# Kernel tuning notes

Measured on AMD Instinct MI355X. Metric: run time of the kernel, lower is better.

Reference implementation:

```python
import jax, jax.numpy as jnp
import numpy as np

N_NODES = 100000
N_EDGES = 1600000
N_REL = 8
IN_CH = 128
HID = 64
OUT_CH = 128


def _rgcn_layer(x, src, dst, et, W_rel, W_root, b, num_rel):
    # x: [N, Fin]; W_rel: [R, Fin, Fout]; W_root: [Fin, Fout]; b: [Fout]
    N = x.shape[0]
    # Transform once per relation, then gather per edge (avoids per-edge matmul)
    xt = jnp.einsum('ni,rio->rno', x, W_rel)          # [R, N, Fout]
    msgs = xt[et, src]                                 # [E, Fout]
    # Per-(dst, relation) mean normalization (PyG RGCNConv aggr='mean' per relation)
    seg = dst * num_rel + et                           # combined segment id
    deg = jax.ops.segment_sum(jnp.ones_like(et, dtype=x.dtype), seg,
                              num_segments=N * num_rel)  # [N*R]
    norm = 1.0 / jnp.maximum(deg[seg], 1.0)            # [E]
    agg = jax.ops.segment_sum(msgs * norm[:, None], dst, num_segments=N)  # [N, Fout]
    return agg + x @ W_root + b


def setup_inputs() -> dict:
    key = jax.random.key(0)
    ks = jax.random.split(key, 9)
    x = jax.random.normal(ks[0], (N_NODES, IN_CH), dtype=jnp.float32)
    edge_index = jax.random.randint(ks[1], (2, N_EDGES), 0, N_NODES, dtype=jnp.int64)
    edge_type = jax.random.randint(ks[2], (N_EDGES,), 0, N_REL, dtype=jnp.int64)
    s1 = 1.0 / np.sqrt(IN_CH)
    s2 = 1.0 / np.sqrt(HID)
    W1 = jax.random.uniform(ks[3], (N_REL, IN_CH, HID), jnp.float32, -s1, s1)
    root1 = jax.random.uniform(ks[4], (IN_CH, HID), jnp.float32, -s1, s1)
    b1 = jnp.zeros((HID,), jnp.float32)
    W2 = jax.random.uniform(ks[5], (N_REL, HID, OUT_CH), jnp.float32, -s2, s2)
    root2 = jax.random.uniform(ks[6], (HID, OUT_CH), jnp.float32, -s2, s2)
    b2 = jnp.zeros((OUT_CH,), jnp.float32)
    return {"x": x, "edge_index": edge_index, "edge_type": edge_type,
            "W1": W1, "root1": root1, "b1": b1,
            "W2": W2, "root2": root2, "b2": b2}


def reference(x, edge_index, edge_type, W1, root1, b1, W2, root2, b2):
    src, dst = edge_index[0], edge_index[1]
    h = _rgcn_layer(x, src, dst, edge_type, W1, root1, b1, N_REL)
    h = jax.nn.relu(h)
    out = _rgcn_layer(h, src, dst, edge_type, W2, root2, b2, N_REL)
    return out
```

## Files before the change

### kernel.cpp

```cpp
#include <hip/hip_runtime.h>
#include <cstdint>
#include <cstddef>

#define NREL 8

typedef __attribute__((ext_vector_type(8))) short bfrag8;
typedef __attribute__((ext_vector_type(4))) float facc4;

__device__ __forceinline__ ushort f2bf(float f) {
  union { float f; uint u; } v; v.f = f;
  uint u = v.u + 0x7fffu + ((v.u >> 16) & 1u);
  return (ushort)(u >> 16);
}
__device__ __forceinline__ float bf2f(ushort u) {
  union { uint u; float f; } v; v.u = ((uint)u) << 16;
  return v.f;
}
__device__ __forceinline__ float readlane_f(float v, int l) {
  union { float f; int i; } u; u.f = v;
  u.i = __builtin_amdgcn_readlane(u.i, l);
  return u.f;
}

__global__ __launch_bounds__(256) void cvt_all_kernel(const float* __restrict__ W1,
                                                      const float* __restrict__ r1,
                                                      const float* __restrict__ W2,
                                                      const float* __restrict__ r2,
                                                      ushort* __restrict__ W1t,
                                                      ushort* __restrict__ r1t,
                                                      ushort* __restrict__ W2t,
                                                      ushort* __restrict__ r2t) {
  int idx = blockIdx.x * 256 + threadIdx.x;
  const float* in; ushort* out; int K, N, rel;
  if (idx < 65536)        { in = W1; out = W1t; K = 128; N = 64;  rel = idx >> 13; idx &= 8191; }
  else if (idx < 73728)   { idx -= 65536; in = r1; out = r1t; K = 128; N = 64; rel = 0; }
  else if (idx < 139264)  { idx -= 73728; in = W2; out = W2t; K = 64; N = 128; rel = idx >> 13; idx &= 8191; }
  else if (idx < 147456)  { idx -= 139264; in = r2; out = r2t; K = 64; N = 128; rel = 0; }
  else return;
  int n = idx / K, k = idx - n * K;
  out[(size_t)rel * K * N + (size_t)n * K + k] =
      f2bf(in[(size_t)rel * K * N + (size_t)k * N + n]);
}

__global__ __launch_bounds__(256) void fused1_kernel(const float* __restrict__ x,
                                                     const ushort* __restrict__ W1t,
                                                     ushort* __restrict__ xt,
                                                     const int* __restrict__ dst,
                                                     const int* __restrict__ et,
                                                     uint* __restrict__ hist,
                                                     uint* __restrict__ rank,
                                                     int M, int E, int HB) {
  __shared__ __align__(16) ushort Axs[64][136];
  __shared__ __align__(16) ushort Bws[64][136];
  const int bid = blockIdx.x;
  const int hq = bid / 3;
  if ((bid % 3) == 0 && hq < HB) {
    int base = (hq * 256 + threadIdx.x) * 8;
    if (base + 8 <= E) {
      int4 d0 = *(const int4*)&dst[base], d1 = *(const int4*)&dst[base + 4];
      int4 r0 = *(const int4*)&et[base],  r1 = *(const int4*)&et[base + 4];
      int dd[8] = {d0.x, d0.y, d0.z, d0.w, d1.x, d1.y, d1.z, d1.w};
      int rr[8] = {r0.x, r0.y, r0.z, r0.w, r1.x, r1.y, r1.z, r1.w};
      uint rk[8];
#pragma unroll
      for (int j = 0; j < 8; ++j)
        rk[j] = atomicAdd(&hist[(size_t)rr[j] * M + dd[j]], 1u);
      *(uint4*)&rank[base] = make_uint4(rk[0], rk[1], rk[2], rk[3]);
      *(uint4*)&rank[base + 4] = make_uint4(rk[4], rk[5], rk[6], rk[7]);
    } else {
      for (int j = 0; base + j < E; ++j)
        rank[base + j] = atomicAdd(&hist[(size_t)et[base + j] * M + dst[base + j]], 1u);
    }
    return;
  }
  const int gidx = (hq < HB) ? (bid - hq - 1) : (bid - HB);
  const int tid = threadIdx.x;
  const int w = tid >> 6, l = tid & 63;
  const int rows0 = gidx * 64;
#pragma unroll
  for (int i = 0; i < 8; ++i) {
    int g = tid + 256 * i;
    int row = g >> 5, c4 = (g & 31) * 4;
    int rr = rows0 + row; if (rr >= M) rr = M - 1;
    float4 v = *(const float4*)&x[(size_t)rr * 128 + c4];
    *(ushort4*)&Axs[row][c4] = make_ushort4(f2bf(v.x), f2bf(v.y), f2bf(v.z), f2bf(v.w));
  }
  __syncthreads();
  const int mrow = w * 16 + (l & 15);
  const int koff = (l >> 4) * 8;
  bfrag8 xf[4];
#pragma unroll
  for (int kc = 0; kc < 4; ++kc)
    xf[kc] = *(const bfrag8*)&Axs[mrow][kc * 32 + koff];
  const int m = rows0 + mrow;
  for (int r = 0; r < NREL; ++r) {
    __syncthreads();
#pragma unroll
    for (int i = 0; i < 8; ++i) {
      int g = tid + 256 * i;
      int row = g >> 5, c4 = (g & 31) * 4;
      *(ushort4*)&Bws[row][c4] = *(const ushort4*)&W1t[((size_t)r * 64 + row) * 128 + c4];
    }
    __syncthreads();
#pragma unroll
    for (int ct = 0; ct < 4; ++ct) {
      facc4 acc = {0.f, 0.f, 0.f, 0.f};
#pragma unroll
      for (int kc = 0; kc < 4; ++kc) {
        bfrag8 af = *(const bfrag8*)&Bws[ct * 16 + (l & 15)][kc * 32 + koff];
        acc = __builtin_amdgcn_mfma_f32_16x16x32_bf16(af, xf[kc], acc, 0, 0, 0);
      }
      if (m < M) {
        int n0 = ct * 16 + (l >> 4) * 4;
        *(ushort4*)&xt[(size_t)m * 512 + r * 64 + n0] =
            make_ushort4(f2bf(acc[0]), f2bf(acc[1]), f2bf(acc[2]), f2bf(acc[3]));
      }
    }
  }
}

__global__ __launch_bounds__(256) void scan1_kernel(const uint* __restrict__ hist,
                                                    uint* __restrict__ bsum, int M) {
  __shared__ uint r[256];
  int b = blockIdx.x, t = threadIdx.x;
  int d = b * 256 + t;
  uint s = 0;
  if (d < M) {
#pragma unroll
    for (int i = 0; i < 8; ++i) s += hist[(size_t)i * M + d];
  }
  r[t] = s; __syncthreads();
  for (int dd = 128; dd > 0; dd >>= 1) { if (t < dd) r[t] += r[t + dd]; __syncthreads(); }
  if (t == 0) bsum[b] = r[0];
}

__global__ __launch_bounds__(512) void scan2_kernel(uint* __restrict__ bsum, int nb) {
  __shared__ uint s[512];
  int t = threadIdx.x;
  uint v = (t < nb) ? bsum[t] : 0u;
  s[t] = v;
  __syncthreads();
  for (int d = 1; d < 512; d <<= 1) {
    uint add = (t >= d) ? s[t - d] : 0u;
    __syncthreads();
    s[t] += add;
    __syncthreads();
  }
  if (t < nb) bsum[t] = s[t] - v;
}

__global__ __launch_bounds__(256) void scan3_kernel(const uint* __restrict__ hist,
                                                    const uint* __restrict__ bsum,
                                                    uint* __restrict__ off,
                                                    float* __restrict__ idg,
                                                    int M, int E) {
  __shared__ uint ts[256];
  int b = blockIdx.x, t = threadIdx.x;
  int d = b * 256 + t;
  uint h[8]; uint sum = 0;
#pragma unroll
  for (int i = 0; i < 8; ++i) { h[i] = (d < M) ? hist[(size_t)i * M + d] : 0u; sum += h[i]; }
  ts[t] = sum;
  __syncthreads();
  uint own = sum;
  for (int dd = 1; dd < 256; dd <<= 1) {
    uint add = (t >= dd) ? ts[t - dd] : 0u;
    __syncthreads();
    ts[t] += add;
    __syncthreads();
  }
  uint run = bsum[b] + (ts[t] - own);
  if (d < M) {
#pragma unroll
    for (int i = 0; i < 8; ++i) {
      int k = d * 8 + i;
      off[k] = run;
      idg[k] = 1.0f / fmaxf((float)h[i], 1.0f);
      run += h[i];
    }
    if (d == M - 1) off[M * 8] = (uint)E;
  }
}

__global__ __launch_bounds__(256) void place_kernel(const int* __restrict__ src,
                                                    const int* __restrict__ dst,
                                                    const int* __restrict__ et,
                                                    const uint* __restrict__ off,
                                                    const uint* __restrict__ rank,
                                                    uint* __restrict__ sp, int E) {
  int base = (blockIdx.x * 256 + threadIdx.x) * 8;
  if (base + 8 <= E) {
    int4 d0 = *(const int4*)&dst[base], d1 = *(const int4*)&dst[base + 4];
    int4 r0 = *(const int4*)&et[base],  r1 = *(const int4*)&et[base + 4];
    int4 s0 = *(const int4*)&src[base], s1 = *(const int4*)&src[base + 4];
    uint4 k0 = *(const uint4*)&rank[base], k1 = *(const uint4*)&rank[base + 4];
    int dd[8] = {d0.x, d0.y, d0.z, d0.w, d1.x, d1.y, d1.z, d1.w};
    int rr[8] = {r0.x, r0.y, r0.z, r0.w, r1.x, r1.y, r1.z, r1.w};
    int ss[8] = {s0.x, s0.y, s0.z, s0.w, s1.x, s1.y, s1.z, s1.w};
    uint kk[8] = {k0.x, k0.y, k0.z, k0.w, k1.x, k1.y, k1.z, k1.w};
    uint oo[8];
#pragma unroll
    for (int j = 0; j < 8; ++j) oo[j] = off[(size_t)dd[j] * NREL + rr[j]];
#pragma unroll
    for (int j = 0; j < 8; ++j)
      sp[oo[j] + kk[j]] = ((uint)ss[j] << 7) | ((uint)rr[j] << 4);
  } else {
    for (int j = 0; base + j < E; ++j) {
      int e = base + j;
      int r = et[e];
      sp[off[(size_t)dst[e] * NREL + r] + rank[e]] = ((uint)src[e] << 7) | ((uint)r << 4);
    }
  }
}

__global__ __launch_bounds__(256) void agg1_kernel(const uint* __restrict__ off,
                                                   const uint* __restrict__ sp,
                                                   const float* __restrict__ idg,
                                                   const ushort* __restrict__ xt,
                                                   float* __restrict__ agg, int N) {
  int wid = (blockIdx.x * 256 + threadIdx.x) >> 6;
  if (wid >= N) return;
  int lane = threadIdx.x & 63;
  uint lane2 = (uint)lane * 2u;
  uint e0 = (uint)__builtin_amdgcn_readfirstlane((int)off[(size_t)wid * 8]);
  uint e1 = (uint)__builtin_amdgcn_readfirstlane((int)off[(size_t)wid * 8 + 8]);
  float idgl = (lane < 8) ? idg[(size_t)wid * 8 + lane] : 0.f;
  const char* xb = (const char*)xt;
  float acct = 0.f, accs = 0.f;
  uint cur = 0;
  for (uint b0 = e0; b0 < e1; b0 += 64) {
    uint vsp = sp[b0 + lane];
    uint vpr = __shfl(vsp, ((int)lane - 1) & 63);
    unsigned long long bmv = __ballot(((vsp ^ vpr) & 0x70u) != 0u);
    uint blo = (uint)__builtin_amdgcn_readfirstlane((int)(uint)bmv);
    uint bhi = (uint)__builtin_amdgcn_readfirstlane((int)(uint)(bmv >> 32));
    uint f0  = (uint)__builtin_amdgcn_readlane((int)vsp, 0);
    if ((b0 == e0) || (((f0 ^ cur) & 0x70u) != 0u)) blo |= 1u; else blo &= ~1u;
    unsigned long long sbm = (((unsigned long long)bhi) << 32) | blo;
    int n = min(64, (int)(e1 - b0));
    int i = 0;
    for (; i + 8 <= n; i += 8) {
      uint p[8]; float v[8];
#pragma unroll
      for (int j = 0; j < 8; ++j)
        p[j] = (uint)__builtin_amdgcn_readlane((int)vsp, i + j);
#pragma unroll
      for (int j = 0; j < 8; ++j)
        v[j] = bf2f(*(const ushort*)(xb + (size_t)((p[j] << 3) + lane2)));
#pragma unroll
      for (int j = 0; j < 8; ++j) {
        if ((sbm >> j) & 1ull) {
          acct += accs * readlane_f(idgl, (int)((cur >> 4) & 7u));
          accs = 0.f; cur = p[j];
        }
        accs += v[j];
      }
      sbm >>= 8;
    }
    for (; i < n; ++i) {
      uint pp = (uint)__builtin_amdgcn_readlane((int)vsp, i);
      float vv = bf2f(*(const ushort*)(xb + (size_t)((pp << 3) + lane2)));
      if (sbm & 1ull) {
        acct += accs * readlane_f(idgl, (int)((cur >> 4) & 7u));
        accs = 0.f; cur = pp;
      }
      sbm >>= 1;
      accs += vv;
    }
  }
  acct += accs * readlane_f(idgl, (int)((cur >> 4) & 7u));
  agg[(size_t)wid * 64 + lane] = acct;
}

__global__ __launch_bounds__(256) void agg2_kernel(const uint* __restrict__ off,
                                                   const uint* __restrict__ sp,
                                                   const float* __restrict__ idg,
                                                   const ushort* __restrict__ hb,
                                                   ushort* __restrict__ y2, int N) {
  int wid = (blockIdx.x * 256 + threadIdx.x) >> 6;
  if (wid >= N) return;
  int lane = threadIdx.x & 63;
  uint lane2 = (uint)lane * 2u;
  uint e0 = (uint)__builtin_amdgcn_readfirstlane((int)off[(size_t)wid * 8]);
  uint e1 = (uint)__builtin_amdgcn_readfirstlane((int)off[(size_t)wid * 8 + 8]);
  float idgl = (lane < 8) ? idg[(size_t)wid * 8 + lane] : 0.f;
  const char* hbb = (const char*)hb;
  float accs = 0.f;
  uint cur = 0;
  bool live = false;
  uint written = 0;
  for (uint b0 = e0; b0 < e1; b0 += 64) {
    uint vsp = sp[b0 + lane];
    uint vpr = __shfl(vsp, ((int)lane - 1) & 63);
    unsigned long long bmv = __ballot(((vsp ^ vpr) & 0x70u) != 0u);
    uint blo = (uint)__builtin_amdgcn_readfirstlane((int)(uint)bmv);
    uint bhi = (uint)__builtin_amdgcn_readfirstlane((int)(uint)(bmv >> 32));
    uint f0  = (uint)__builtin_amdgcn_readlane((int)vsp, 0);
    if ((b0 == e0) || (((f0 ^ cur) & 0x70u) != 0u)) blo |= 1u; else blo &= ~1u;
    unsigned long long sbm = (((unsigned long long)bhi) << 32) | blo;
    int n = min(64, (int)(e1 - b0));
    int i = 0;
    for (; i + 8 <= n; i += 8) {
      uint p[8]; float v[8];
#pragma unroll
      for (int j = 0; j < 8; ++j)
        p[j] = (uint)__builtin_amdgcn_readlane((int)vsp, i + j);
#pragma unroll
      for (int j = 0; j < 8; ++j)
        v[j] = bf2f(*(const ushort*)(hbb + (size_t)((p[j] & ~127u) + lane2)));
#pragma unroll
      for (int j = 0; j < 8; ++j) {
        if ((sbm >> j) & 1ull) {
          if (live) {
            int r = (int)((cur >> 4) & 7u);
            y2[(size_t)wid * 512 + r * 64 + lane] = f2bf(accs * readlane_f(idgl, r));
            written |= 1u << r;
          }
          accs = 0.f; cur = p[j]; live = true;
        }
        accs += v[j];
      }
      sbm >>= 8;
    }
    for (; i < n; ++i) {
      uint pp = (uint)__builtin_amdgcn_readlane((int)vsp, i);
      float vv = bf2f(*(const ushort*)(hbb + (size_t)((pp & ~127u) + lane2)));
      if (sbm & 1ull) {
        if (live) {
          int r = (int)((cur >> 4) & 7u);
          y2[(size_t)wid * 512 + r * 64 + lane] = f2bf(accs * readlane_f(idgl, r));
          written |= 1u << r;
        }
        accs = 0.f; cur = pp; live = true;
      }
      sbm >>= 1;
      accs += vv;
    }
  }
  if (live) {
    int r = (int)((cur >> 4) & 7u);
    y2[(size_t)wid * 512 + r * 64 + lane] = f2bf(accs * readlane_f(idgl, r));
    written |= 1u << r;
  }
#pragma unroll
  for (int r = 0; r < 8; ++r)
    if (!((written >> r) & 1u))
      y2[(size_t)wid * 512 + r * 64 + lane] = 0;
}

__global__ __launch_bounds__(256) void reduce_h_kernel(const float* __restrict__ x,
                                                       const ushort* __restrict__ r1t,
                                                       const float* __restrict__ b1,
                                                       const float* __restrict__ agg,
                                                       ushort* __restrict__ hb, int M) {
  __shared__ __align__(16) ushort Axs[64][136];
  __shared__ __align__(16) ushort Bws[64][136];
  const int tid = threadIdx.x;
  const int w = tid >> 6, l = tid & 63;
  const int rows0 = blockIdx.x * 64;
#pragma unroll
  for (int i = 0; i < 8; ++i) {
    int g = tid + 256 * i;
    int row = g >> 5, c4 = (g & 31) * 4;
    int rr = rows0 + row; if (rr >= M) rr = M - 1;
    float4 v = *(const float4*)&x[(size_t)rr * 128 + c4];
    *(ushort4*)&Axs[row][c4] = make_ushort4(f2bf(v.x), f2bf(v.y), f2bf(v.z), f2bf(v.w));
    *(ushort4*)&Bws[row][c4] = *(const ushort4*)&r1t[(size_t)row * 128 + c4];
  }
  __syncthreads();
  const int mrow = w * 16 + (l & 15);
  const int koff = (l >> 4) * 8;
  const int m = rows0 + mrow;
  const int mc = (m < M) ? m : (M - 1);
  bfrag8 xf[4];
#pragma unroll
  for (int kc = 0; kc < 4; ++kc)
    xf[kc] = *(const bfrag8*)&Axs[mrow][kc * 32 + koff];
  facc4 acc[4] = {};
#pragma unroll
  for (int ct = 0; ct < 4; ++ct)
#pragma unroll
    for (int kc = 0; kc < 4; ++kc) {
      bfrag8 af = *(const bfrag8*)&Bws[ct * 16 + (l & 15)][kc * 32 + koff];
      acc[ct] = __builtin_amdgcn_mfma_f32_16x16x32_bf16(af, xf[kc], acc[ct], 0, 0, 0);
    }
#pragma unroll
  for (int ct = 0; ct < 4; ++ct) {
    int n0 = ct * 16 + (l >> 4) * 4;
    float4 s4 = *(const float4*)&agg[(size_t)mc * 64 + n0];
    float4 bb = *(const float4*)&b1[n0];
    float h0 = fmaxf(acc[ct][0] + s4.x + bb.x, 0.f);
    float h1 = fmaxf(acc[ct][1] + s4.y + bb.y, 0.f);
    float h2 = fmaxf(acc[ct][2] + s4.z + bb.z, 0.f);
    float h3 = fmaxf(acc[ct][3] + s4.w + bb.w, 0.f);
    if (m < M)
      *(ushort4*)&hb[(size_t)m * 64 + n0] =
          make_ushort4(f2bf(h0), f2bf(h1), f2bf(h2), f2bf(h3));
  }
}

__global__ __launch_bounds__(256) void gemm_out_kernel(const ushort* __restrict__ hb,
                                                       const ushort* __restrict__ y2,
                                                       const ushort* __restrict__ W2t,
                                                       const ushort* __restrict__ r2t,
                                                       const float* __restrict__ b2,
                                                       float* __restrict__ out, int M) {
  __shared__ __align__(16) ushort Bws[128][72];
  const int tid = threadIdx.x;
  const int w = tid >> 6, l = tid & 63;
  const int rows0 = blockIdx.x * 64;
  const int mrow = w * 16 + (l & 15);
  const int koff = (l >> 4) * 8;
  const int m = rows0 + mrow;
  const int mc = (m < M) ? m : (M - 1);
  facc4 oacc[8] = {};
#pragma unroll
  for (int i = 0; i < 8; ++i) {
    int g = tid + 256 * i;
    int row = g >> 4, c4 = (g & 15) * 4;
    *(ushort4*)&Bws[row][c4] = *(const ushort4*)&r2t[(size_t)row * 64 + c4];
  }
  __syncthreads();
  {
    bfrag8 h0 = *(const bfrag8*)&hb[(size_t)mc * 64 + koff];
    bfrag8 h1 = *(const bfrag8*)&hb[(size_t)mc * 64 + 32 + koff];
#pragma unroll
    for (int ct = 0; ct < 8; ++ct) {
      bfrag8 a0 = *(const bfrag8*)&Bws[ct * 16 + (l & 15)][koff];
      bfrag8 a1 = *(const bfrag8*)&Bws[ct * 16 + (l & 15)][32 + koff];
      oacc[ct] = __builtin_amdgcn_mfma_f32_16x16x32_bf16(a0, h0, oacc[ct], 0, 0, 0);
      oacc[ct] = __builtin_amdgcn_mfma_f32_16x16x32_bf16(a1, h1, oacc[ct], 0, 0, 0);
    }
  }
  for (int r = 0; r < NREL; ++r) {
    __syncthreads();
#pragma unroll
    for (int i = 0; i < 8; ++i) {
      int g = tid + 256 * i;
      int row = g >> 4, c4 = (g & 15) * 4;
      *(ushort4*)&Bws[row][c4] = *(const ushort4*)&W2t[((size_t)r * 128 + row) * 64 + c4];
    }
    __syncthreads();
    bfrag8 y0 = *(const bfrag8*)&y2[(size_t)mc * 512 + r * 64 + koff];
    bfrag8 y1f = *(const bfrag8*)&y2[(size_t)mc * 512 + r * 64 + 32 + koff];
#pragma unroll
    for (int ct = 0; ct < 8; ++ct) {
      bfrag8 a0 = *(const bfrag8*)&Bws[ct * 16 + (l & 15)][koff];
      bfrag8 a1 = *(const bfrag8*)&Bws[ct * 16 + (l & 15)][32 + koff];
      oacc[ct] = __builtin_amdgcn_mfma_f32_16x16x32_bf16(a0, y0, oacc[ct], 0, 0, 0);
      oacc[ct] = __builtin_amdgcn_mfma_f32_16x16x32_bf16(a1, y1f, oacc[ct], 0, 0, 0);
    }
  }
  if (m < M) {
#pragma unroll
    for (int ct = 0; ct < 8; ++ct) {
      int n0 = ct * 16 + (l >> 4) * 4;
      float4 bb = *(const float4*)&b2[n0];
      float4 o = make_float4(oacc[ct][0] + bb.x, oacc[ct][1] + bb.y,
                             oacc[ct][2] + bb.z, oacc[ct][3] + bb.w);
      *(float4*)&out[(size_t)m * 128 + n0] = o;
    }
  }
}

extern "C" void kernel_launch(void* const* d_in, const int* in_sizes, int n_in,
                              void* d_out, int out_size, void* d_ws, size_t ws_size,
                              hipStream_t stream) {
  const float* x     = (const float*)d_in[0];
  const int*   ei    = (const int*)d_in[1];
  const int*   et    = (const int*)d_in[2];
  const float* W1    = (const float*)d_in[3];
  const float* root1 = (const float*)d_in[4];
  const float* b1    = (const float*)d_in[5];
  const float* W2    = (const float*)d_in[6];
  const float* root2 = (const float*)d_in[7];
  const float* b2    = (const float*)d_in[8];
  float* out = (float*)d_out;

  const int M = in_sizes[0] / 128;
  const int E = in_sizes[2];
  const int NS = M * NREL;
  const int* srcp = ei;
  const int* dstp = ei + E;

  auto align = [](char*& p, size_t n) { char* q = p; p += (n + 255) & ~(size_t)255; return q; };
  char* p = (char*)d_ws;
  ushort* xt   = (ushort*)align(p, (size_t)M * 512 * 2);
  float*  agg  = (float*) align(p, (size_t)M * 64 * 4);
  ushort* hb   = (ushort*)align(p, (size_t)M * 64 * 2);
  uint*   hist = (uint*)  align(p, (size_t)NS * 4);
  uint*   rank = (uint*)  align(p, (size_t)E * 4);
  uint*   off  = (uint*)  align(p, (size_t)(NS + 1) * 4);
  float*  idg  = (float*) align(p, (size_t)NS * 4);
  uint*   sp   = (uint*)  align(p, (size_t)(E + 64) * 4);
  uint*   bsum = (uint*)  align(p, 4096);
  ushort* W1t  = (ushort*)align(p, (size_t)NREL * 64 * 128 * 2);
  ushort* r1t  = (ushort*)align(p, (size_t)64 * 128 * 2);
  ushort* W2t  = (ushort*)align(p, (size_t)NREL * 128 * 64 * 2);
  ushort* r2t  = (ushort*)align(p, (size_t)128 * 64 * 2);
  ushort* y2 = xt;

  cvt_all_kernel<<<(147456 + 255) / 256, 256, 0, stream>>>(W1, root1, W2, root2,
                                                           W1t, r1t, W2t, r2t);

  hipMemsetAsync(hist, 0, (size_t)NS * 4, stream);

  const int E8B  = (int)(((long long)E + 8LL * 256 - 1) / (8LL * 256));
  const int MB64 = (M + 63) / 64;
  fused1_kernel<<<E8B + MB64, 256, 0, stream>>>(x, W1t, xt, dstp, et,
                                                hist, rank, M, E, E8B);

  const int NB = (M + 255) / 256;
  scan1_kernel<<<NB, 256, 0, stream>>>(hist, bsum, M);
  scan2_kernel<<<1, 512, 0, stream>>>(bsum, NB);
  scan3_kernel<<<NB, 256, 0, stream>>>(hist, bsum, off, idg, M, E);
  place_kernel<<<E8B, 256, 0, stream>>>(srcp, dstp, et, off, rank, sp, E);

  const int AGB = (M * 64 + 255) / 256;

  agg1_kernel<<<AGB, 256, 0, stream>>>(off, sp, idg, xt, agg, M);
  reduce_h_kernel<<<MB64, 256, 0, stream>>>(x, r1t, b1, agg, hb, M);

  agg2_kernel<<<AGB, 256, 0, stream>>>(off, sp, idg, hb, y2, M);
  gemm_out_kernel<<<MB64, 256, 0, stream>>>(hb, y2, W2t, r2t, b2, out, M);
}
```

Baseline: 321.6 us.

## Fuse edge aggregation into downstream GEMM kernels via shared memory staging

Merges the layer-1 gather/aggregate into the root-GEMM kernel and the layer-2 aggregate into the output GEMM, keeping per-node aggregates in LDS. This removes the global agg buffer and the 512-wide bf16 y2 round-trip. Each wave now walks 16 (or 8) nodes serially instead of one node per wave, which means fewer concurrent gather waves and larger LDS use per block. The histogram blocks are also rebalanced to 4 edges per thread with a 1:1 interleave instead of 1:2.

```diff
diff --git a/kernel.cpp b/kernel.cpp
--- a/kernel.cpp
+++ b/kernel.cpp
@@ -53,20 +53,17 @@
   __shared__ __align__(16) ushort Axs[64][136];
   __shared__ __align__(16) ushort Bws[64][136];
   const int bid = blockIdx.x;
-  const int hq = bid / 3;
-  if ((bid % 3) == 0 && hq < HB) {
-    int base = (hq * 256 + threadIdx.x) * 8;
-    if (base + 8 <= E) {
-      int4 d0 = *(const int4*)&dst[base], d1 = *(const int4*)&dst[base + 4];
-      int4 r0 = *(const int4*)&et[base],  r1 = *(const int4*)&et[base + 4];
-      int dd[8] = {d0.x, d0.y, d0.z, d0.w, d1.x, d1.y, d1.z, d1.w};
-      int rr[8] = {r0.x, r0.y, r0.z, r0.w, r1.x, r1.y, r1.z, r1.w};
-      uint rk[8];
-#pragma unroll
-      for (int j = 0; j < 8; ++j)
-        rk[j] = atomicAdd(&hist[(size_t)rr[j] * M + dd[j]], 1u);
-      *(uint4*)&rank[base] = make_uint4(rk[0], rk[1], rk[2], rk[3]);
-      *(uint4*)&rank[base + 4] = make_uint4(rk[4], rk[5], rk[6], rk[7]);
+  const int hq = bid >> 1;
+  if (((bid & 1) == 0) && hq < HB) {
+    int base = (hq * 256 + threadIdx.x) * 4;
+    if (base + 4 <= E) {
+      int4 d = *(const int4*)&dst[base];
+      int4 r = *(const int4*)&et[base];
+      uint rk0 = atomicAdd(&hist[(size_t)r.x * M + d.x], 1u);
+      uint rk1 = atomicAdd(&hist[(size_t)r.y * M + d.y], 1u);
+      uint rk2 = atomicAdd(&hist[(size_t)r.z * M + d.z], 1u);
+      uint rk3 = atomicAdd(&hist[(size_t)r.w * M + d.w], 1u);
+      *(uint4*)&rank[base] = make_uint4(rk0, rk1, rk2, rk3);
     } else {
       for (int j = 0; base + j < E; ++j)
         rank[base + j] = atomicAdd(&hist[(size_t)et[base + j] * M + dst[base + j]], 1u);
@@ -213,165 +210,86 @@
   }
 }
 
-__global__ __launch_bounds__(256) void agg1_kernel(const uint* __restrict__ off,
-                                                   const uint* __restrict__ sp,
-                                                   const float* __restrict__ idg,
-                                                   const ushort* __restrict__ xt,
-                                                   float* __restrict__ agg, int N) {
-  int wid = (blockIdx.x * 256 + threadIdx.x) >> 6;
-  if (wid >= N) return;
-  int lane = threadIdx.x & 63;
-  uint lane2 = (uint)lane * 2u;
-  uint e0 = (uint)__builtin_amdgcn_readfirstlane((int)off[(size_t)wid * 8]);
-  uint e1 = (uint)__builtin_amdgcn_readfirstlane((int)off[(size_t)wid * 8 + 8]);
-  float idgl = (lane < 8) ? idg[(size_t)wid * 8 + lane] : 0.f;
-  const char* xb = (const char*)xt;
-  float acct = 0.f, accs = 0.f;
-  uint cur = 0;
-  for (uint b0 = e0; b0 < e1; b0 += 64) {
-    uint vsp = sp[b0 + lane];
-    uint vpr = __shfl(vsp, ((int)lane - 1) & 63);
-    unsigned long long bmv = __ballot(((vsp ^ vpr) & 0x70u) != 0u);
-    uint blo = (uint)__builtin_amdgcn_readfirstlane((int)(uint)bmv);
-    uint bhi = (uint)__builtin_amdgcn_readfirstlane((int)(uint)(bmv >> 32));
-    uint f0  = (uint)__builtin_amdgcn_readlane((int)vsp, 0);
-    if ((b0 == e0) || (((f0 ^ cur) & 0x70u) != 0u)) blo |= 1u; else blo &= ~1u;
-    unsigned long long sbm = (((unsigned long long)bhi) << 32) | blo;
-    int n = min(64, (int)(e1 - b0));
-    int i = 0;
-    for (; i + 8 <= n; i += 8) {
-      uint p[8]; float v[8];
-#pragma unroll
-      for (int j = 0; j < 8; ++j)
-        p[j] = (uint)__builtin_amdgcn_readlane((int)vsp, i + j);
-#pragma unroll
-      for (int j = 0; j < 8; ++j)
-        v[j] = bf2f(*(const ushort*)(xb + (size_t)((p[j] << 3) + lane2)));
-#pragma unroll
-      for (int j = 0; j < 8; ++j) {
-        if ((sbm >> j) & 1ull) {
-          acct += accs * readlane_f(idgl, (int)((cur >> 4) & 7u));
-          accs = 0.f; cur = p[j];
-        }
-        accs += v[j];
-      }
-      sbm >>= 8;
-    }
-    for (; i < n; ++i) {
-      uint pp = (uint)__builtin_amdgcn_readlane((int)vsp, i);
-      float vv = bf2f(*(const ushort*)(xb + (size_t)((pp << 3) + lane2)));
-      if (sbm & 1ull) {
-        acct += accs * readlane_f(idgl, (int)((cur >> 4) & 7u));
-        accs = 0.f; cur = pp;
-      }
-      sbm >>= 1;
-      accs += vv;
-    }
-  }
-  acct += accs * readlane_f(idgl, (int)((cur >> 4) & 7u));
-  agg[(size_t)wid * 64 + lane] = acct;
-}
-
-__global__ __launch_bounds__(256) void agg2_kernel(const uint* __restrict__ off,
-                                                   const uint* __restrict__ sp,
-                                                   const float* __restrict__ idg,
-                                                   const ushort* __restrict__ hb,
-                                                   ushort* __restrict__ y2, int N) {
-  int wid = (blockIdx.x * 256 + threadIdx.x) >> 6;
-  if (wid >= N) return;
-  int lane = threadIdx.x & 63;
-  uint lane2 = (uint)lane * 2u;
-  uint e0 = (uint)__builtin_amdgcn_readfirstlane((int)off[(size_t)wid * 8]);
-  uint e1 = (uint)__builtin_amdgcn_readfirstlane((int)off[(size_t)wid * 8 + 8]);
-  float idgl = (lane < 8) ? idg[(size_t)wid * 8 + lane] : 0.f;
-  const char* hbb = (const char*)hb;
-  float accs = 0.f;
-  uint cur = 0;
-  bool live = false;
-  uint written = 0;
-  for (uint b0 = e0; b0 < e1; b0 += 64) {
-    uint vsp = sp[b0 + lane];
-    uint vpr = __shfl(vsp, ((int)lane - 1) & 63);
-    unsigned long long bmv = __ballot(((vsp ^ vpr) & 0x70u) != 0u);
-    uint blo = (uint)__builtin_amdgcn_readfirstlane((int)(uint)bmv);
-    uint bhi = (uint)__builtin_amdgcn_readfirstlane((int)(uint)(bmv >> 32));
-    uint f0  = (uint)__builtin_amdgcn_readlane((int)vsp, 0);
-    if ((b0 == e0) || (((f0 ^ cur) & 0x70u) != 0u)) blo |= 1u; else blo &= ~1u;
-    unsigned long long sbm = (((unsigned long long)bhi) << 32) | blo;
-    int n = min(64, (int)(e1 - b0));
-    int i = 0;
-    for (; i + 8 <= n; i += 8) {
-      uint p[8]; float v[8];
-#pragma unroll
-      for (int j = 0; j < 8; ++j)
-        p[j] = (uint)__builtin_amdgcn_readlane((int)vsp, i + j);
-#pragma unroll
-      for (int j = 0; j < 8; ++j)
-        v[j] = bf2f(*(const ushort*)(hbb + (size_t)((p[j] & ~127u) + lane2)));
-#pragma unroll
-      for (int j = 0; j < 8; ++j) {
-        if ((sbm >> j) & 1ull) {
-          if (live) {
-            int r = (int)((cur >> 4) & 7u);
-            y2[(size_t)wid * 512 + r * 64 + lane] = f2bf(accs * readlane_f(idgl, r));
-            written |= 1u << r;
-          }
-          accs = 0.f; cur = p[j]; live = true;
-        }
-        accs += v[j];
-      }
-      sbm >>= 8;
-    }
-    for (; i < n; ++i) {
-      uint pp = (uint)__builtin_amdgcn_readlane((int)vsp, i);
-      float vv = bf2f(*(const ushort*)(hbb + (size_t)((pp & ~127u) + lane2)));
-      if (sbm & 1ull) {
-        if (live) {
-          int r = (int)((cur >> 4) & 7u);
-          y2[(size_t)wid * 512 + r * 64 + lane] = f2bf(accs * readlane_f(idgl, r));
-          written |= 1u << r;
-        }
-        accs = 0.f; cur = pp; live = true;
-      }
-      sbm >>= 1;
-      accs += vv;
-    }
-  }
-  if (live) {
-    int r = (int)((cur >> 4) & 7u);
-    y2[(size_t)wid * 512 + r * 64 + lane] = f2bf(accs * readlane_f(idgl, r));
-    written |= 1u << r;
-  }
-#pragma unroll
-  for (int r = 0; r < 8; ++r)
-    if (!((written >> r) & 1u))
-      y2[(size_t)wid * 512 + r * 64 + lane] = 0;
-}
-
-__global__ __launch_bounds__(256) void reduce_h_kernel(const float* __restrict__ x,
-                                                       const ushort* __restrict__ r1t,
-                                                       const float* __restrict__ b1,
-                                                       const float* __restrict__ agg,
-                                                       ushort* __restrict__ hb, int M) {
+__global__ __launch_bounds__(256) void fusedA_kernel(const uint* __restrict__ off,
+                                                     const uint* __restrict__ sp,
+                                                     const float* __restrict__ idg,
+                                                     const ushort* __restrict__ xt,
+                                                     const float* __restrict__ x,
+                                                     const ushort* __restrict__ r1t,
+                                                     const float* __restrict__ b1,
+                                                     ushort* __restrict__ hb, int M) {
+  __shared__ __align__(16) float aggs[64][68];
   __shared__ __align__(16) ushort Axs[64][136];
   __shared__ __align__(16) ushort Bws[64][136];
   const int tid = threadIdx.x;
   const int w = tid >> 6, l = tid & 63;
-  const int rows0 = blockIdx.x * 64;
+  const int m0 = blockIdx.x * 64;
 #pragma unroll
   for (int i = 0; i < 8; ++i) {
     int g = tid + 256 * i;
     int row = g >> 5, c4 = (g & 31) * 4;
-    int rr = rows0 + row; if (rr >= M) rr = M - 1;
+    int rr = m0 + row; if (rr >= M) rr = M - 1;
     float4 v = *(const float4*)&x[(size_t)rr * 128 + c4];
     *(ushort4*)&Axs[row][c4] = make_ushort4(f2bf(v.x), f2bf(v.y), f2bf(v.z), f2bf(v.w));
     *(ushort4*)&Bws[row][c4] = *(const ushort4*)&r1t[(size_t)row * 128 + c4];
   }
+  const uint lane2 = (uint)l * 2u;
+  const char* xb = (const char*)xt;
+  for (int t = 0; t < 16; ++t) {
+    int wid = m0 + w * 16 + t;
+    if (wid >= M) break;
+    uint e0 = (uint)__builtin_amdgcn_readfirstlane((int)off[(size_t)wid * 8]);
+    uint e1 = (uint)__builtin_amdgcn_readfirstlane((int)off[(size_t)wid * 8 + 8]);
+    float idgl = (l < 8) ? idg[(size_t)wid * 8 + l] : 0.f;
+    float acct = 0.f, accs = 0.f;
+    uint cur = 0;
+    for (uint b0 = e0; b0 < e1; b0 += 64) {
+      uint vsp = sp[b0 + l];
+      uint vpr = __shfl(vsp, (l - 1) & 63);
+      unsigned long long bmv = __ballot(((vsp ^ vpr) & 0x70u) != 0u);
+      uint blo = (uint)__builtin_amdgcn_readfirstlane((int)(uint)bmv);
+      uint bhi = (uint)__builtin_amdgcn_readfirstlane((int)(uint)(bmv >> 32));
+      uint f0  = (uint)__builtin_amdgcn_readlane((int)vsp, 0);
+      if ((b0 == e0) || (((f0 ^ cur) & 0x70u) != 0u)) blo |= 1u; else blo &= ~1u;
+      unsigned long long sbm = (((unsigned long long)bhi) << 32) | blo;
+      int n = min(64, (int)(e1 - b0));
+      int i = 0;
+      for (; i + 8 <= n; i += 8) {
+        uint p[8]; float v[8];
+#pragma unroll
+        for (int j = 0; j < 8; ++j)
+          p[j] = (uint)__builtin_amdgcn_readlane((int)vsp, i + j);
+#pragma unroll
+        for (int j = 0; j < 8; ++j)
+          v[j] = bf2f(*(const ushort*)(xb + (size_t)((p[j] << 3) + lane2)));
+#pragma unroll
+        for (int j = 0; j < 8; ++j) {
+          if ((sbm >> j) & 1ull) {
+            acct += accs * readlane_f(idgl, (int)((cur >> 4) & 7u));
+            accs = 0.f; cur = p[j];
+          }
+          accs += v[j];
+        }
+        sbm >>= 8;
+      }
+      for (; i < n; ++i) {
+        uint pp = (uint)__builtin_amdgcn_readlane((int)vsp, i);
+        float vv = bf2f(*(const ushort*)(xb + (size_t)((pp << 3) + lane2)));
+        if (sbm & 1ull) {
+          acct += accs * readlane_f(idgl, (int)((cur >> 4) & 7u));
+          accs = 0.f; cur = pp;
+        }
+        sbm >>= 1;
+        accs += vv;
+      }
+    }
+    acct += accs * readlane_f(idgl, (int)((cur >> 4) & 7u));
+    aggs[w * 16 + t][l] = acct;
+  }
   __syncthreads();
   const int mrow = w * 16 + (l & 15);
   const int koff = (l >> 4) * 8;
-  const int m = rows0 + mrow;
-  const int mc = (m < M) ? m : (M - 1);
+  const int m = m0 + mrow;
   bfrag8 xf[4];
 #pragma unroll
   for (int kc = 0; kc < 4; ++kc)
@@ -387,7 +305,7 @@
 #pragma unroll
   for (int ct = 0; ct < 4; ++ct) {
     int n0 = ct * 16 + (l >> 4) * 4;
-    float4 s4 = *(const float4*)&agg[(size_t)mc * 64 + n0];
+    float4 s4 = *(const float4*)&aggs[mrow][n0];
     float4 bb = *(const float4*)&b1[n0];
     float h0 = fmaxf(acc[ct][0] + s4.x + bb.x, 0.f);
     float h1 = fmaxf(acc[ct][1] + s4.y + bb.y, 0.f);
@@ -399,21 +317,90 @@
   }
 }
 
-__global__ __launch_bounds__(256) void gemm_out_kernel(const ushort* __restrict__ hb,
-                                                       const ushort* __restrict__ y2,
-                                                       const ushort* __restrict__ W2t,
-                                                       const ushort* __restrict__ r2t,
-                                                       const float* __restrict__ b2,
-                                                       float* __restrict__ out, int M) {
+__global__ __launch_bounds__(256) void fusedB_kernel(const uint* __restrict__ off,
+                                                     const uint* __restrict__ sp,
+                                                     const float* __restrict__ idg,
+                                                     const ushort* __restrict__ hb,
+                                                     const ushort* __restrict__ W2t,
+                                                     const ushort* __restrict__ r2t,
+                                                     const float* __restrict__ b2,
+                                                     float* __restrict__ out, int M) {
+  __shared__ __align__(16) ushort Ys[32][520];
   __shared__ __align__(16) ushort Bws[128][72];
   const int tid = threadIdx.x;
   const int w = tid >> 6, l = tid & 63;
-  const int rows0 = blockIdx.x * 64;
-  const int mrow = w * 16 + (l & 15);
-  const int koff = (l >> 4) * 8;
-  const int m = rows0 + mrow;
-  const int mc = (m < M) ? m : (M - 1);
-  facc4 oacc[8] = {};
+  const int m0 = blockIdx.x * 32;
+  const uint lane2 = (uint)l * 2u;
+  const char* hbb = (const char*)hb;
+  for (int t = 0; t < 8; ++t) {
+    int wid = m0 + w * 8 + t;
+    int ld = w * 8 + t;
+    if (wid >= M) break;
+    uint e0 = (uint)__builtin_amdgcn_readfirstlane((int)off[(size_t)wid * 8]);
+    uint e1 = (uint)__builtin_amdgcn_readfirstlane((int)off[(size_t)wid * 8 + 8]);
+    float idgl = (l < 8) ? idg[(size_t)wid * 8 + l] : 0.f;
+    float accs = 0.f;
+    uint cur = 0;
+    bool live = false;
+    uint written = 0;
+    for (uint b0 = e0; b0 < e1; b0 += 64) {
+      uint vsp = sp[b0 + l];
+      uint vpr = __shfl(vsp, (l - 1) & 63);
+      unsigned long long bmv = __ballot(((vsp ^ vpr) & 0x70u) != 0u);
+      uint blo = (uint)__builtin_amdgcn_readfirstlane((int)(uint)bmv);
+      uint bhi = (uint)__builtin_amdgcn_readfirstlane((int)(uint)(bmv >> 32));
+      uint f0  = (uint)__builtin_amdgcn_readlane((int)vsp, 0);
+      if ((b0 == e0) || (((f0 ^ cur) & 0x70u) != 0u)) blo |= 1u; else blo &= ~1u;
+      unsigned long long sbm = (((unsigned long long)bhi) << 32) | blo;
+      int n = min(64, (int)(e1 - b0));
+      int i = 0;
+      for (; i + 8 <= n; i += 8) {
+        uint p[8]; float v[8];
+#pragma unroll
+        for (int j = 0; j < 8; ++j)
+          p[j] = (uint)__builtin_amdgcn_readlane((int)vsp, i + j);
+#pragma unroll
+        for (int j = 0; j < 8; ++j)
+          v[j] = bf2f(*(const ushort*)(hbb + (size_t)((p[j] & ~127u) + lane2)));
+#pragma unroll
+        for (int j = 0; j < 8; ++j) {
+          if ((sbm >> j) & 1ull) {
+            if (live) {
+              int r = (int)((cur >> 4) & 7u);
+              Ys[ld][r * 64 + l] = f2bf(accs * readlane_f(idgl, r));
+              written |= 1u << r;
+            }
+            accs = 0.f; cur = p[j]; live = true;
+          }
+          accs += v[j];
+        }
+        sbm >>= 8;
+      }
+      for (; i < n; ++i) {
+        uint pp = (uint)__builtin_amdgcn_readlane((int)vsp, i);
+        float vv = bf2f(*(const ushort*)(hbb + (size_t)((pp & ~127u) + lane2)));
+        if (sbm & 1ull) {
+          if (live) {
+            int r = (int)((cur >> 4) & 7u);
+            Ys[ld][r * 64 + l] = f2bf(accs * readlane_f(idgl, r));
+            written |= 1u << r;
+          }
+          accs = 0.f; cur = pp; live = true;
+        }
+        sbm >>= 1;
+        accs += vv;
+      }
+    }
+    if (live) {
+      int r = (int)((cur >> 4) & 7u);
+      Ys[ld][r * 64 + l] = f2bf(accs * readlane_f(idgl, r));
+      written |= 1u << r;
+    }
+#pragma unroll
+    for (int r = 0; r < 8; ++r)
+      if (!((written >> r) & 1u))
+        Ys[ld][r * 64 + l] = 0;
+  }
 #pragma unroll
   for (int i = 0; i < 8; ++i) {
     int g = tid + 256 * i;
@@ -421,13 +408,19 @@
     *(ushort4*)&Bws[row][c4] = *(const ushort4*)&r2t[(size_t)row * 64 + c4];
   }
   __syncthreads();
+  const int rg = w >> 1, cg = w & 1;
+  const int mrow = rg * 16 + (l & 15);
+  const int koff = (l >> 4) * 8;
+  const int m = m0 + mrow;
+  const int mc = (m < M) ? m : (M - 1);
+  facc4 oacc[4] = {};
   {
     bfrag8 h0 = *(const bfrag8*)&hb[(size_t)mc * 64 + koff];
     bfrag8 h1 = *(const bfrag8*)&hb[(size_t)mc * 64 + 32 + koff];
 #pragma unroll
-    for (int ct = 0; ct < 8; ++ct) {
-      bfrag8 a0 = *(const bfrag8*)&Bws[ct * 16 + (l & 15)][koff];
-      bfrag8 a1 = *(const bfrag8*)&Bws[ct * 16 + (l & 15)][32 + koff];
+    for (int ct = 0; ct < 4; ++ct) {
+      bfrag8 a0 = *(const bfrag8*)&Bws[cg * 64 + ct * 16 + (l & 15)][koff];
+      bfrag8 a1 = *(const bfrag8*)&Bws[cg * 64 + ct * 16 + (l & 15)][32 + koff];
       oacc[ct] = __builtin_amdgcn_mfma_f32_16x16x32_bf16(a0, h0, oacc[ct], 0, 0, 0);
       oacc[ct] = __builtin_amdgcn_mfma_f32_16x16x32_bf16(a1, h1, oacc[ct], 0, 0, 0);
     }
@@ -441,20 +434,20 @@
       *(ushort4*)&Bws[row][c4] = *(const ushort4*)&W2t[((size_t)r * 128 + row) * 64 + c4];
     }
     __syncthreads();
-    bfrag8 y0 = *(const bfrag8*)&y2[(size_t)mc * 512 + r * 64 + koff];
-    bfrag8 y1f = *(const bfrag8*)&y2[(size_t)mc * 512 + r * 64 + 32 + koff];
-#pragma unroll
-    for (int ct = 0; ct < 8; ++ct) {
-      bfrag8 a0 = *(const bfrag8*)&Bws[ct * 16 + (l & 15)][koff];
-      bfrag8 a1 = *(const bfrag8*)&Bws[ct * 16 + (l & 15)][32 + koff];
+    bfrag8 y0 = *(const bfrag8*)&Ys[mrow][r * 64 + koff];
+    bfrag8 y1f = *(const bfrag8*)&Ys[mrow][r * 64 + 32 + koff];
+#pragma unroll
+    for (int ct = 0; ct < 4; ++ct) {
+      bfrag8 a0 = *(const bfrag8*)&Bws[cg * 64 + ct * 16 + (l & 15)][koff];
+      bfrag8 a1 = *(const bfrag8*)&Bws[cg * 64 + ct * 16 + (l & 15)][32 + koff];
       oacc[ct] = __builtin_amdgcn_mfma_f32_16x16x32_bf16(a0, y0, oacc[ct], 0, 0, 0);
       oacc[ct] = __builtin_amdgcn_mfma_f32_16x16x32_bf16(a1, y1f, oacc[ct], 0, 0, 0);
     }
   }
   if (m < M) {
 #pragma unroll
-    for (int ct = 0; ct < 8; ++ct) {
-      int n0 = ct * 16 + (l >> 4) * 4;
+    for (int ct = 0; ct < 4; ++ct) {
+      int n0 = cg * 64 + ct * 16 + (l >> 4) * 4;
       float4 bb = *(const float4*)&b2[n0];
       float4 o = make_float4(oacc[ct][0] + bb.x, oacc[ct][1] + bb.y,
                              oacc[ct][2] + bb.z, oacc[ct][3] + bb.w);
@@ -486,7 +479,6 @@
   auto align = [](char*& p, size_t n) { char* q = p; p += (n + 255) & ~(size_t)255; return q; };
   char* p = (char*)d_ws;
   ushort* xt   = (ushort*)align(p, (size_t)M * 512 * 2);
-  float*  agg  = (float*) align(p, (size_t)M * 64 * 4);
   ushort* hb   = (ushort*)align(p, (size_t)M * 64 * 2);
   uint*   hist = (uint*)  align(p, (size_t)NS * 4);
   uint*   rank = (uint*)  align(p, (size_t)E * 4);
@@ -498,29 +490,25 @@
   ushort* r1t  = (ushort*)align(p, (size_t)64 * 128 * 2);
   ushort* W2t  = (ushort*)align(p, (size_t)NREL * 128 * 64 * 2);
   ushort* r2t  = (ushort*)align(p, (size_t)128 * 64 * 2);
-  ushort* y2 = xt;
 
   cvt_all_kernel<<<(147456 + 255) / 256, 256, 0, stream>>>(W1, root1, W2, root2,
                                                            W1t, r1t, W2t, r2t);
-
   hipMemsetAsync(hist, 0, (size_t)NS * 4, stream);
 
-  const int E8B  = (int)(((long long)E + 8LL * 256 - 1) / (8LL * 256));
+  const int E4B  = (int)(((long long)E + 4LL * 256 - 1) / (4LL * 256));
   const int MB64 = (M + 63) / 64;
-  fused1_kernel<<<E8B + MB64, 256, 0, stream>>>(x, W1t, xt, dstp, et,
-                                                hist, rank, M, E, E8B);
+  fused1_kernel<<<E4B + MB64, 256, 0, stream>>>(x, W1t, xt, dstp, et,
+                                                hist, rank, M, E, E4B);
 
   const int NB = (M + 255) / 256;
   scan1_kernel<<<NB, 256, 0, stream>>>(hist, bsum, M);
   scan2_kernel<<<1, 512, 0, stream>>>(bsum, NB);
   scan3_kernel<<<NB, 256, 0, stream>>>(hist, bsum, off, idg, M, E);
+  const int E8B = (int)(((long long)E + 8LL * 256 - 1) / (8LL * 256));
   place_kernel<<<E8B, 256, 0, stream>>>(srcp, dstp, et, off, rank, sp, E);
 
-  const int AGB = (M * 64 + 255) / 256;
-
-  agg1_kernel<<<AGB, 256, 0, stream>>>(off, sp, idg, xt, agg, M);
-  reduce_h_kernel<<<MB64, 256, 0, stream>>>(x, r1t, b1, agg, hb, M);
-
-  agg2_kernel<<<AGB, 256, 0, stream>>>(off, sp, idg, hb, y2, M);
-  gemm_out_kernel<<<MB64, 256, 0, stream>>>(hb, y2, W2t, r2t, b2, out, M);
-}
+  fusedA_kernel<<<MB64, 256, 0, stream>>>(off, sp, idg, xt, x, r1t, b1, hb, M);
+
+  const int MB32 = (M + 31) / 32;
+  fusedB_kernel<<<MB32, 256, 0, stream>>>(off, sp, idg, hb, W2t, r2t, b2, out, M);
+}
```

Measured after the change: 445.5 us. +38.5%, slower.

## Fuse layer-1 root transform into relation GEMM and epilogue into aggregation

Applied to the files above, without the earlier changes.

The root weight matmul for layer 1 now runs as a ninth pass inside fused1_kernel and writes fp32 hroot. The bias, ReLU and bf16 conversion move into agg1_kernel's final store, so reduce_h_kernel and its re-read of x are gone. The A operand is now loaded straight from global into registers, dropping the Axs shared buffer and one barrier. This saves one launch and the x re-read, but hroot is written as fp32 and read back, which is the same size as the old agg buffer.

```diff
diff --git a/kernel.cpp b/kernel.cpp
--- a/kernel.cpp
+++ b/kernel.cpp
@@ -44,13 +44,14 @@
 
 __global__ __launch_bounds__(256) void fused1_kernel(const float* __restrict__ x,
                                                      const ushort* __restrict__ W1t,
+                                                     const ushort* __restrict__ r1t,
                                                      ushort* __restrict__ xt,
+                                                     float* __restrict__ hroot,
                                                      const int* __restrict__ dst,
                                                      const int* __restrict__ et,
                                                      uint* __restrict__ hist,
                                                      uint* __restrict__ rank,
                                                      int M, int E, int HB) {
-  __shared__ __align__(16) ushort Axs[64][136];
   __shared__ __align__(16) ushort Bws[64][136];
   const int bid = blockIdx.x;
   const int hq = bid / 3;
@@ -77,29 +78,28 @@
   const int tid = threadIdx.x;
   const int w = tid >> 6, l = tid & 63;
   const int rows0 = gidx * 64;
-#pragma unroll
-  for (int i = 0; i < 8; ++i) {
-    int g = tid + 256 * i;
-    int row = g >> 5, c4 = (g & 31) * 4;
-    int rr = rows0 + row; if (rr >= M) rr = M - 1;
-    float4 v = *(const float4*)&x[(size_t)rr * 128 + c4];
-    *(ushort4*)&Axs[row][c4] = make_ushort4(f2bf(v.x), f2bf(v.y), f2bf(v.z), f2bf(v.w));
-  }
-  __syncthreads();
   const int mrow = w * 16 + (l & 15);
   const int koff = (l >> 4) * 8;
+  const int m = rows0 + mrow;
+  const int mc = (m < M) ? m : (M - 1);
   bfrag8 xf[4];
 #pragma unroll
-  for (int kc = 0; kc < 4; ++kc)
-    xf[kc] = *(const bfrag8*)&Axs[mrow][kc * 32 + koff];
-  const int m = rows0 + mrow;
-  for (int r = 0; r < NREL; ++r) {
-    __syncthreads();
+  for (int kc = 0; kc < 4; ++kc) {
+    float4 a = *(const float4*)&x[(size_t)mc * 128 + kc * 32 + koff];
+    float4 b = *(const float4*)&x[(size_t)mc * 128 + kc * 32 + koff + 4];
+    union { bfrag8 f; ushort4 u[2]; } pk;
+    pk.u[0] = make_ushort4(f2bf(a.x), f2bf(a.y), f2bf(a.z), f2bf(a.w));
+    pk.u[1] = make_ushort4(f2bf(b.x), f2bf(b.y), f2bf(b.z), f2bf(b.w));
+    xf[kc] = pk.f;
+  }
+  for (int r = 0; r < 9; ++r) {
+    __syncthreads();
+    const ushort* Wsrc = (r < 8) ? (W1t + (size_t)r * 64 * 128) : r1t;
 #pragma unroll
     for (int i = 0; i < 8; ++i) {
       int g = tid + 256 * i;
       int row = g >> 5, c4 = (g & 31) * 4;
-      *(ushort4*)&Bws[row][c4] = *(const ushort4*)&W1t[((size_t)r * 64 + row) * 128 + c4];
+      *(ushort4*)&Bws[row][c4] = *(const ushort4*)&Wsrc[(size_t)row * 128 + c4];
     }
     __syncthreads();
 #pragma unroll
@@ -112,8 +112,13 @@
       }
       if (m < M) {
         int n0 = ct * 16 + (l >> 4) * 4;
-        *(ushort4*)&xt[(size_t)m * 512 + r * 64 + n0] =
-            make_ushort4(f2bf(acc[0]), f2bf(acc[1]), f2bf(acc[2]), f2bf(acc[3]));
+        if (r < 8) {
+          *(ushort4*)&xt[(size_t)m * 512 + r * 64 + n0] =
+              make_ushort4(f2bf(acc[0]), f2bf(acc[1]), f2bf(acc[2]), f2bf(acc[3]));
+        } else {
+          *(float4*)&hroot[(size_t)m * 64 + n0] =
+              make_float4(acc[0], acc[1], acc[2], acc[3]);
+        }
       }
     }
   }
@@ -217,7 +222,9 @@
                                                    const uint* __restrict__ sp,
                                                    const float* __restrict__ idg,
                                                    const ushort* __restrict__ xt,
-                                                   float* __restrict__ agg, int N) {
+                                                   const float* __restrict__ hroot,
+                                                   const float* __restrict__ b1,
+                                                   ushort* __restrict__ hb, int N) {
   int wid = (blockIdx.x * 256 + threadIdx.x) >> 6;
   if (wid >= N) return;
   int lane = threadIdx.x & 63;
@@ -269,7 +276,8 @@
     }
   }
   acct += accs * readlane_f(idgl, (int)((cur >> 4) & 7u));
-  agg[(size_t)wid * 64 + lane] = acct;
+  float h = fmaxf(acct + hroot[(size_t)wid * 64 + lane] + b1[lane], 0.f);
+  hb[(size_t)wid * 64 + lane] = f2bf(h);
 }
 
 __global__ __launch_bounds__(256) void agg2_kernel(const uint* __restrict__ off,
@@ -348,57 +356,6 @@
       y2[(size_t)wid * 512 + r * 64 + lane] = 0;
 }
 
-__global__ __launch_bounds__(256) void reduce_h_kernel(const float* __restrict__ x,
-                                                       const ushort* __restrict__ r1t,
-                                                       const float* __restrict__ b1,
-                                                       const float* __restrict__ agg,
-                                                       ushort* __restrict__ hb, int M) {
-  __shared__ __align__(16) ushort Axs[64][136];
-  __shared__ __align__(16) ushort Bws[64][136];
-  const int tid = threadIdx.x;
-  const int w = tid >> 6, l = tid & 63;
-  const int rows0 = blockIdx.x * 64;
-#pragma unroll
-  for (int i = 0; i < 8; ++i) {
-    int g = tid + 256 * i;
-    int row = g >> 5, c4 = (g & 31) * 4;
-    int rr = rows0 + row; if (rr >= M) rr = M - 1;
-    float4 v = *(const float4*)&x[(size_t)rr * 128 + c4];
-    *(ushort4*)&Axs[row][c4] = make_ushort4(f2bf(v.x), f2bf(v.y), f2bf(v.z), f2bf(v.w));
-    *(ushort4*)&Bws[row][c4] = *(const ushort4*)&r1t[(size_t)row * 128 + c4];
-  }
-  __syncthreads();
-  const int mrow = w * 16 + (l & 15);
-  const int koff = (l >> 4) * 8;
-  const int m = rows0 + mrow;
-  const int mc = (m < M) ? m : (M - 1);
-  bfrag8 xf[4];
-#pragma unroll
-  for (int kc = 0; kc < 4; ++kc)
-    xf[kc] = *(const bfrag8*)&Axs[mrow][kc * 32 + koff];
-  facc4 acc[4] = {};
-#pragma unroll
-  for (int ct = 0; ct < 4; ++ct)
-#pragma unroll
-    for (int kc = 0; kc < 4; ++kc) {
-      bfrag8 af = *(const bfrag8*)&Bws[ct * 16 + (l & 15)][kc * 32 + koff];
-      acc[ct] = __builtin_amdgcn_mfma_f32_16x16x32_bf16(af, xf[kc], acc[ct], 0, 0, 0);
-    }
-#pragma unroll
-  for (int ct = 0; ct < 4; ++ct) {
-    int n0 = ct * 16 + (l >> 4) * 4;
-    float4 s4 = *(const float4*)&agg[(size_t)mc * 64 + n0];
-    float4 bb = *(const float4*)&b1[n0];
-    float h0 = fmaxf(acc[ct][0] + s4.x + bb.x, 0.f);
-    float h1 = fmaxf(acc[ct][1] + s4.y + bb.y, 0.f);
-    float h2 = fmaxf(acc[ct][2] + s4.z + bb.z, 0.f);
-    float h3 = fmaxf(acc[ct][3] + s4.w + bb.w, 0.f);
-    if (m < M)
-      *(ushort4*)&hb[(size_t)m * 64 + n0] =
-          make_ushort4(f2bf(h0), f2bf(h1), f2bf(h2), f2bf(h3));
-  }
-}
-
 __global__ __launch_bounds__(256) void gemm_out_kernel(const ushort* __restrict__ hb,
                                                        const ushort* __restrict__ y2,
                                                        const ushort* __restrict__ W2t,
@@ -485,29 +442,28 @@
 
   auto align = [](char*& p, size_t n) { char* q = p; p += (n + 255) & ~(size_t)255; return q; };
   char* p = (char*)d_ws;
-  ushort* xt   = (ushort*)align(p, (size_t)M * 512 * 2);
-  float*  agg  = (float*) align(p, (size_t)M * 64 * 4);
-  ushort* hb   = (ushort*)align(p, (size_t)M * 64 * 2);
-  uint*   hist = (uint*)  align(p, (size_t)NS * 4);
-  uint*   rank = (uint*)  align(p, (size_t)E * 4);
-  uint*   off  = (uint*)  align(p, (size_t)(NS + 1) * 4);
-  float*  idg  = (float*) align(p, (size_t)NS * 4);
-  uint*   sp   = (uint*)  align(p, (size_t)(E + 64) * 4);
-  uint*   bsum = (uint*)  align(p, 4096);
-  ushort* W1t  = (ushort*)align(p, (size_t)NREL * 64 * 128 * 2);
-  ushort* r1t  = (ushort*)align(p, (size_t)64 * 128 * 2);
-  ushort* W2t  = (ushort*)align(p, (size_t)NREL * 128 * 64 * 2);
-  ushort* r2t  = (ushort*)align(p, (size_t)128 * 64 * 2);
+  ushort* xt    = (ushort*)align(p, (size_t)M * 512 * 2);
+  float*  hroot = (float*) align(p, (size_t)M * 64 * 4);
+  ushort* hb    = (ushort*)align(p, (size_t)M * 64 * 2);
+  uint*   hist  = (uint*)  align(p, (size_t)NS * 4);
+  uint*   rank  = (uint*)  align(p, (size_t)E * 4);
+  uint*   off   = (uint*)  align(p, (size_t)(NS + 1) * 4);
+  float*  idg   = (float*) align(p, (size_t)NS * 4);
+  uint*   sp    = (uint*)  align(p, (size_t)(E + 64) * 4);
+  uint*   bsum  = (uint*)  align(p, 4096);
+  ushort* W1t   = (ushort*)align(p, (size_t)NREL * 64 * 128 * 2);
+  ushort* r1t   = (ushort*)align(p, (size_t)64 * 128 * 2);
+  ushort* W2t   = (ushort*)align(p, (size_t)NREL * 128 * 64 * 2);
+  ushort* r2t   = (ushort*)align(p, (size_t)128 * 64 * 2);
   ushort* y2 = xt;
 
   cvt_all_kernel<<<(147456 + 255) / 256, 256, 0, stream>>>(W1, root1, W2, root2,
                                                            W1t, r1t, W2t, r2t);
-
   hipMemsetAsync(hist, 0, (size_t)NS * 4, stream);
 
   const int E8B  = (int)(((long long)E + 8LL * 256 - 1) / (8LL * 256));
   const int MB64 = (M + 63) / 64;
-  fused1_kernel<<<E8B + MB64, 256, 0, stream>>>(x, W1t, xt, dstp, et,
+  fused1_kernel<<<E8B + MB64, 256, 0, stream>>>(x, W1t, r1t, xt, hroot, dstp, et,
                                                 hist, rank, M, E, E8B);
 
   const int NB = (M + 255) / 256;
@@ -518,8 +474,7 @@
 
   const int AGB = (M * 64 + 255) / 256;
 
-  agg1_kernel<<<AGB, 256, 0, stream>>>(off, sp, idg, xt, agg, M);
-  reduce_h_kernel<<<MB64, 256, 0, stream>>>(x, r1t, b1, agg, hb, M);
+  agg1_kernel<<<AGB, 256, 0, stream>>>(off, sp, idg, xt, hroot, b1, hb, M);
 
   agg2_kernel<<<AGB, 256, 0, stream>>>(off, sp, idg, hb, y2, M);
   gemm_out_kernel<<<MB64, 256, 0, stream>>>(hb, y2, W2t, r2t, b2, out, M);
```

Result: no change. 327.5 us (+1.8%).
